# Optimization experiments

Measured on AMD Instinct MI355X. Metric: run time of the kernel, lower is better.

Reference implementation:

```python
import jax, jax.numpy as jnp
import numpy as np

HIDDEN = 8
RES = 64
BS = 2048


def totalistic(x):
    # D4-symmetrize the 5x5 kernels over spatial dims, then remove per-kernel spatial mean
    z = 0.125 * (x + x[:, :, ::-1, :] + x[:, :, :, ::-1] + x[:, :, ::-1, ::-1])
    xt = jnp.swapaxes(x, 2, 3)
    z = z + 0.125 * (xt + xt[:, :, ::-1, :] + xt[:, :, :, ::-1] + xt[:, :, ::-1, ::-1])
    return z - z.mean(axis=(2, 3), keepdims=True)


def setup_inputs() -> dict:
    key = jax.random.key(0)
    k0, k1, k2, k3, k4, k5 = jax.random.split(key, 6)
    psi = jax.random.uniform(k0, (BS, HIDDEN, RES, RES), jnp.float32) * 2.0 - 1.0
    filter1 = jax.random.normal(k1, (HIDDEN, 1, 5, 5), jnp.float32)
    bias1 = jnp.zeros((HIDDEN,), jnp.float32)  # initialized as 0*randn in torch
    fan = 1.0 / np.sqrt(HIDDEN).astype(np.float32)
    w2 = jax.random.uniform(k2, (HIDDEN, HIDDEN), jnp.float32, -fan, fan)
    b2 = jax.random.uniform(k3, (HIDDEN,), jnp.float32, -fan, fan)
    w3 = jax.random.uniform(k4, (HIDDEN, HIDDEN), jnp.float32, -fan, fan)
    b3 = jax.random.uniform(k5, (HIDDEN,), jnp.float32, -fan, fan)
    return {"psi": psi, "filter1": filter1, "bias1": bias1,
            "w2": w2, "b2": b2, "w3": w3, "b3": b3}


def reference(psi, filter1, bias1, w2, b2, w3, b3):
    # depthwise 5x5 conv with D4-symmetrized, zero-mean kernel; padding=2 (SAME)
    w = totalistic(filter1)  # [H,1,5,5]
    z = jax.lax.conv_general_dilated(
        psi, w, window_strides=(1, 1), padding=[(2, 2), (2, 2)],
        dimension_numbers=("NCHW", "OIHW", "NCHW"), feature_group_count=HIDDEN)
    z = z + bias1[None, :, None, None]
    z = jax.nn.leaky_relu(z)  # default negative_slope 0.01, matches torch
    # 1x1 pointwise conv == per-pixel 8x8 GEMM
    z = jax.nn.leaky_relu(jnp.einsum("oi,bihw->bohw", w2, z) + b2[None, :, None, None])
    out = jnp.tanh(psi + jnp.einsum("oi,bihw->bohw", w3, z) + b3[None, :, None, None])
    return out
```

## Files before the change

kernel.cpp:

```cpp
#include <hip/hip_runtime.h>
#include <hip/hip_fp16.h>


#define HIDDEN 8
#define RES    64
#define SLAB   16
#define SROWS  20
#define SSTR2  35
#define ZSTR2  33

__global__ __launch_bounds__(256, 4)
void ca_fused(const float* __restrict__ psi,
              const float* __restrict__ filter1,
              const float* __restrict__ bias1,
              const float* __restrict__ w2,
              const float* __restrict__ b2,
              const float* __restrict__ w3,
              const float* __restrict__ b3,
              float* __restrict__ out)
{
    __shared__ __half2 s_in[HIDDEN * SROWS * SSTR2];
    __shared__ __half2 s_z [HIDDEN * SLAB  * ZSTR2];
    __shared__ float   s_coef[HIDDEN * 8];

    const int tid  = threadIdx.x;
    const int b    = blockIdx.x >> 2;
    const int slab = blockIdx.x & 3;
    const int y0   = slab * SLAB;

    const float* psib = psi + (size_t)b * (HIDDEN * RES * RES);

    if (tid < HIDDEN) {
        const float* f = filter1 + tid * 25;
        float x[25];
        float m = 0.f;
        #pragma unroll
        for (int i = 0; i < 25; ++i) { x[i] = f[i]; m += x[i]; }
        m *= 0.04f;
        float A = x[12] - m;
        float B = 0.25f  * (x[7]+x[17]+x[11]+x[13]) - m;
        float C = 0.25f  * (x[6]+x[8]+x[16]+x[18]) - m;
        float D = 0.25f  * (x[2]+x[22]+x[10]+x[14]) - m;
        float E = 0.125f * (x[1]+x[3]+x[21]+x[23]+x[5]+x[15]+x[9]+x[19]) - m;
        float F = 0.25f  * (x[0]+x[4]+x[20]+x[24]) - m;
        s_coef[tid*8+0] = A; s_coef[tid*8+1] = B; s_coef[tid*8+2] = C;
        s_coef[tid*8+3] = D; s_coef[tid*8+4] = E; s_coef[tid*8+5] = F;
        s_coef[tid*8+6] = bias1[tid];
    }

    for (int p = tid; p < HIDDEN * SROWS * 34; p += 256) {
        int c   = p / (SROWS * 34);
        int rem = p - c * (SROWS * 34);
        int r   = rem / 34;
        int px  = rem - r * 34;
        int gy  = y0 - 2 + r;
        float2 v = make_float2(0.f, 0.f);
        if ((unsigned)gy < RES && px >= 1 && px <= 32)
            v = *(const float2*)(psib + ((c << 12) | (gy << 6)) + (2*px - 2));
        s_in[(c * SROWS + r) * SSTR2 + px] = __floats2half2_rn(v.x, v.y);
    }
    __syncthreads();

    #pragma unroll
    for (int jj = 0; jj < 2; ++jj) {
        int job = tid + (jj << 8);
        int c   = job >> 6;
        int y   = (job >> 2) & 15;
        int seg = job & 3;
        int base = (c * SROWS + y) * SSTR2 + (seg << 3);

        float r0[20], r1[20], r2[20];
        #pragma unroll
        for (int k = 0; k < 10; ++k) {
            __half2 p0 = s_in[base              + k];
            __half2 p1 = s_in[base +   SSTR2    + k];
            __half2 p2 = s_in[base + 2*SSTR2    + k];
            __half2 p3 = s_in[base + 3*SSTR2    + k];
            __half2 p4 = s_in[base + 4*SSTR2    + k];
            __half2 v1 = __hadd2(p1, p3);
            __half2 v2 = __hadd2(p0, p4);
            float2 f0 = __half22float2(p2);
            float2 f1 = __half22float2(v1);
            float2 f2 = __half22float2(v2);
            r0[2*k] = f0.x; r0[2*k+1] = f0.y;
            r1[2*k] = f1.x; r1[2*k+1] = f1.y;
            r2[2*k] = f2.x; r2[2*k+1] = f2.y;
        }
        float A  = s_coef[c*8+0], Bc = s_coef[c*8+1], Cc = s_coef[c*8+2];
        float Dc = s_coef[c*8+3], Ec = s_coef[c*8+4], Fc = s_coef[c*8+5];
        float bias = s_coef[c*8+6];

        int zbase = (c * SLAB + y) * ZSTR2 + (seg << 3);
        #pragma unroll
        for (int j2 = 0; j2 < 8; ++j2) {
            float vv[2];
            #pragma unroll
            for (int t = 0; t < 2; ++t) {
                int j = 2*j2 + t;
                float v = A  *  r0[j+2]
                        + Bc * (r0[j+1] + r0[j+3] + r1[j+2])
                        + Cc * (r1[j+1] + r1[j+3])
                        + Dc * (r0[j]   + r0[j+4] + r2[j+2])
                        + Ec * (r1[j]   + r1[j+4] + r2[j+1] + r2[j+3])
                        + Fc * (r2[j]   + r2[j+4])
                        + bias;
                vv[t] = fmaxf(v, 0.01f * v);
            }
            s_z[zbase + j2] = __floats2half2_rn(vv[0], vv[1]);
        }
    }
    __syncthreads();

    float* outb = out + (size_t)b * (HIDDEN * RES * RES);
    #pragma unroll
    for (int gg = 0; gg < 2; ++gg) {
        int q  = tid + (gg << 8);
        int y  = q >> 5;
        int xh = q & 31;

        float za[8], zb_[8];
        #pragma unroll
        for (int c = 0; c < 8; ++c) {
            float2 f = __half22float2(s_z[(c * SLAB + y) * ZSTR2 + xh]);
            za[c] = f.x; zb_[c] = f.y;
        }
        float ha[8], hb[8];
        #pragma unroll
        for (int o = 0; o < 8; ++o) {
            float a0 = b2[o], a1 = a0;
            #pragma unroll
            for (int i = 0; i < 8; ++i) {
                float w = w2[o*8+i];
                a0 = fmaf(w, za[i],  a0);
                a1 = fmaf(w, zb_[i], a1);
            }
            ha[o] = fmaxf(a0, 0.01f * a0);
            hb[o] = fmaxf(a1, 0.01f * a1);
        }
        #pragma unroll
        for (int o = 0; o < 8; ++o) {
            float g0 = b3[o], g1 = g0;
            #pragma unroll
            for (int i = 0; i < 8; ++i) {
                float w = w3[o*8+i];
                g0 = fmaf(w, ha[i], g0);
                g1 = fmaf(w, hb[i], g1);
            }
            float2 ps = __half22float2(s_in[(o * SROWS + y + 2) * SSTR2 + xh + 1]);
            float t0 = ps.x + g0;
            float t1 = ps.y + g1;
            float e0 = __expf(2.f * t0);
            float e1 = __expf(2.f * t1);
            float o0 = 1.f - 2.f * __builtin_amdgcn_rcpf(e0 + 1.f);
            float o1 = 1.f - 2.f * __builtin_amdgcn_rcpf(e1 + 1.f);
            *(float2*)(outb + (o << 12) + ((y0 + y) << 6) + 2*xh) = make_float2(o0, o1);
        }
    }
}

extern "C" void kernel_launch(void* const* d_in, const int* in_sizes, int n_in,
                              void* d_out, int out_size, void* d_ws, size_t ws_size,
                              hipStream_t stream) {
    const float* psi     = (const float*)d_in[0];
    const float* filter1 = (const float*)d_in[1];
    const float* bias1   = (const float*)d_in[2];
    const float* w2      = (const float*)d_in[3];
    const float* b2      = (const float*)d_in[4];
    const float* w3      = (const float*)d_in[5];
    const float* b3      = (const float*)d_in[6];
    float* out = (float*)d_out;

    dim3 grid(2048 * 4);
    dim3 block(256);
    hipLaunchKernelGGL(ca_fused, grid, block, 0, stream,
                       psi, filter1, bias1, w2, b2, w3, b3, out);
}
```

Before: 546.4 us.

## Halve slab height, double grid and occupancy, use packed float2 math

```diff
diff --git a/kernel.cpp b/kernel.cpp
--- a/kernel.cpp
+++ b/kernel.cpp
@@ -4,12 +4,16 @@
 
 #define HIDDEN 8
 #define RES    64
-#define SLAB   16
-#define SROWS  20
+#define SLAB   8
+#define SROWS  12
 #define SSTR2  35
 #define ZSTR2  33
 
-__global__ __launch_bounds__(256, 4)
+typedef float v2f __attribute__((ext_vector_type(2)));
+
+#define PV(a, i) ((v2f){ (a)[(i)], (a)[(i) + 1] })
+
+__global__ __launch_bounds__(256, 8)
 void ca_fused(const float* __restrict__ psi,
               const float* __restrict__ filter1,
               const float* __restrict__ bias1,
@@ -24,8 +28,8 @@
     __shared__ float   s_coef[HIDDEN * 8];
 
     const int tid  = threadIdx.x;
-    const int b    = blockIdx.x >> 2;
-    const int slab = blockIdx.x & 3;
+    const int b    = blockIdx.x >> 3;
+    const int slab = blockIdx.x & 7;
     const int y0   = slab * SLAB;
 
     const float* psib = psi + (size_t)b * (HIDDEN * RES * RES);
@@ -61,13 +65,11 @@
     }
     __syncthreads();
 
-    #pragma unroll
-    for (int jj = 0; jj < 2; ++jj) {
-        int job = tid + (jj << 8);
-        int c   = job >> 6;
-        int y   = (job >> 2) & 15;
-        int seg = job & 3;
-        int base = (c * SROWS + y) * SSTR2 + (seg << 3);
+    {
+        const int c   = tid >> 5;
+        const int y   = (tid >> 2) & 7;
+        const int seg = tid & 3;
+        const int base = (c * SROWS + y) * SSTR2 + (seg << 3);
 
         float r0[20], r1[20], r2[20];
         #pragma unroll
@@ -90,65 +92,56 @@
         float Dc = s_coef[c*8+3], Ec = s_coef[c*8+4], Fc = s_coef[c*8+5];
         float bias = s_coef[c*8+6];
 
-        int zbase = (c * SLAB + y) * ZSTR2 + (seg << 3);
+        const int zbase = (c * SLAB + y) * ZSTR2 + (seg << 3);
         #pragma unroll
         for (int j2 = 0; j2 < 8; ++j2) {
-            float vv[2];
-            #pragma unroll
-            for (int t = 0; t < 2; ++t) {
-                int j = 2*j2 + t;
-                float v = A  *  r0[j+2]
-                        + Bc * (r0[j+1] + r0[j+3] + r1[j+2])
-                        + Cc * (r1[j+1] + r1[j+3])
-                        + Dc * (r0[j]   + r0[j+4] + r2[j+2])
-                        + Ec * (r1[j]   + r1[j+4] + r2[j+1] + r2[j+3])
-                        + Fc * (r2[j]   + r2[j+4])
-                        + bias;
-                vv[t] = fmaxf(v, 0.01f * v);
-            }
-            s_z[zbase + j2] = __floats2half2_rn(vv[0], vv[1]);
+            const int j = 2 * j2;
+            v2f v = A  * PV(r0, j+2)
+                  + Bc * (PV(r0, j+1) + PV(r0, j+3) + PV(r1, j+2))
+                  + Cc * (PV(r1, j+1) + PV(r1, j+3))
+                  + Dc * (PV(r0, j)   + PV(r0, j+4) + PV(r2, j+2))
+                  + Ec * (PV(r1, j)   + PV(r1, j+4) + PV(r2, j+1) + PV(r2, j+3))
+                  + Fc * (PV(r2, j)   + PV(r2, j+4))
+                  + bias;
+            v2f w = 0.01f * v;
+            s_z[zbase + j2] = __floats2half2_rn(fmaxf(v.x, w.x), fmaxf(v.y, w.y));
         }
     }
     __syncthreads();
 
     float* outb = out + (size_t)b * (HIDDEN * RES * RES);
-    #pragma unroll
-    for (int gg = 0; gg < 2; ++gg) {
-        int q  = tid + (gg << 8);
-        int y  = q >> 5;
-        int xh = q & 31;
+    {
+        const int q  = tid;
+        const int y  = q >> 5;
+        const int xh = q & 31;
 
-        float za[8], zb_[8];
+        v2f z2[8];
         #pragma unroll
         for (int c = 0; c < 8; ++c) {
             float2 f = __half22float2(s_z[(c * SLAB + y) * ZSTR2 + xh]);
-            za[c] = f.x; zb_[c] = f.y;
+            z2[c] = (v2f){f.x, f.y};
         }
-        float ha[8], hb[8];
+        v2f h2[8];
         #pragma unroll
         for (int o = 0; o < 8; ++o) {
-            float a0 = b2[o], a1 = a0;
+            float bb = b2[o];
+            v2f a = (v2f){bb, bb};
             #pragma unroll
-            for (int i = 0; i < 8; ++i) {
-                float w = w2[o*8+i];
-                a0 = fmaf(w, za[i],  a0);
-                a1 = fmaf(w, zb_[i], a1);
-            }
-            ha[o] = fmaxf(a0, 0.01f * a0);
-            hb[o] = fmaxf(a1, 0.01f * a1);
+            for (int i = 0; i < 8; ++i)
+                a += w2[o*8+i] * z2[i];
+            v2f t = 0.01f * a;
+            h2[o] = (v2f){fmaxf(a.x, t.x), fmaxf(a.y, t.y)};
         }
         #pragma unroll
         for (int o = 0; o < 8; ++o) {
-            float g0 = b3[o], g1 = g0;
+            float bb = b3[o];
+            v2f g = (v2f){bb, bb};
             #pragma unroll
-            for (int i = 0; i < 8; ++i) {
-                float w = w3[o*8+i];
-                g0 = fmaf(w, ha[i], g0);
-                g1 = fmaf(w, hb[i], g1);
-            }
+            for (int i = 0; i < 8; ++i)
+                g += w3[o*8+i] * h2[i];
             float2 ps = __half22float2(s_in[(o * SROWS + y + 2) * SSTR2 + xh + 1]);
-            float t0 = ps.x + g0;
-            float t1 = ps.y + g1;
+            float t0 = ps.x + g.x;
+            float t1 = ps.y + g.y;
             float e0 = __expf(2.f * t0);
             float e1 = __expf(2.f * t1);
             float o0 = 1.f - 2.f * __builtin_amdgcn_rcpf(e0 + 1.f);
@@ -170,7 +163,7 @@
     const float* b3      = (const float*)d_in[6];
     float* out = (float*)d_out;
 
-    dim3 grid(2048 * 4);
+    dim3 grid(2048 * 8);
     dim3 block(256);
     hipLaunchKernelGGL(ca_fused, grid, block, 0, stream,
                        psi, filter1, bias1, w2, b2, w3, b3, out);
```

New measurement: 489.9 us. 10.3% less time.
